# Optimization experiments

Hardware: AMD Instinct MI355X
Metric: run time of the kernel (lower is better)

The kernel has to match this reference:

```python
import jax, jax.numpy as jnp
import numpy as np

WS = 8            # window_size
SHIFT = WS // 2   # cyclic shift
NHEADS = 6
EPS = 1e-5


def _rel_pos_index(ws):
    coords = np.stack(np.meshgrid(np.arange(ws), np.arange(ws), indexing='ij'))  # [2,ws,ws]
    flat = coords.reshape(2, -1)                       # [2,N]
    rel = flat[:, :, None] - flat[:, None, :]          # [2,N,N]
    rel = rel.transpose(1, 2, 0).copy()
    rel[:, :, 0] += ws - 1
    rel[:, :, 1] += ws - 1
    rel[:, :, 0] *= 2 * ws - 1
    return rel.sum(-1)                                 # [N,N] indices into bias table


def _attn_mask(H, W, ws, shift):
    # standard Swin boundary mask for the shifted configuration
    img = np.zeros((H, W))
    cnt = 0
    for hs in (slice(0, -ws), slice(-ws, -shift), slice(-shift, None)):
        for wsl in (slice(0, -ws), slice(-ws, -shift), slice(-shift, None)):
            img[hs, wsl] = cnt
            cnt += 1
    mw = img.reshape(H // ws, ws, W // ws, ws).transpose(0, 2, 1, 3).reshape(-1, ws * ws)
    m = mw[:, None, :] - mw[:, :, None]
    return np.where(m != 0, -100.0, 0.0).astype(np.float32)  # [nW, N, N]


def instance_norm(x):
    # InstanceNorm over spatial dims, no affine (torch default)
    m = x.mean(axis=(2, 3), keepdims=True)
    v = x.var(axis=(2, 3), keepdims=True)
    return (x - m) * jax.lax.rsqrt(v + EPS)


def setup_inputs() -> dict:
    key = jax.random.key(0)
    ks = jax.random.split(key, 8)
    B, C, H, W, E = 4, 192, 256, 256, 128
    s = 0.02
    return {
        'x': jax.random.normal(ks[0], (B, C, H, W), jnp.float32),
        'cond': jax.random.normal(ks[1], (B, E), jnp.float32),
        'qkv_w': jax.random.normal(ks[2], (3 * C, C), jnp.float32) * s,
        'qkv_b': jnp.zeros((3 * C,), jnp.float32),
        'proj_w': jax.random.normal(ks[3], (C, C), jnp.float32) * s,
        'proj_b': jnp.zeros((C,), jnp.float32),
        'rel_bias': jax.random.normal(ks[4], ((2 * WS - 1) ** 2, NHEADS), jnp.float32) * s,
        'film_w': jax.random.normal(ks[5], (2 * C, E), jnp.float32) * s,
        'film_b': jnp.zeros((2 * C,), jnp.float32),
    }


def shifted_window_attention(xn, qkv_w, qkv_b, proj_w, proj_b, rel_bias):
    B, C, H, W = xn.shape
    h, ws, shift = NHEADS, WS, SHIFT
    d = C // h
    N = ws * ws
    nW = (H // ws) * (W // ws)
    scale = d ** -0.5

    xs = jnp.transpose(xn, (0, 2, 3, 1))                         # BHWC
    xs = jnp.roll(xs, (-shift, -shift), axis=(1, 2))             # cyclic shift
    win = xs.reshape(B, H // ws, ws, W // ws, ws, C)
    win = win.transpose(0, 1, 3, 2, 4, 5).reshape(B * nW, N, C)  # window partition

    qkv = win @ qkv_w.T + qkv_b                                  # [Bn, N, 3C]
    q, k, v = [t.reshape(B * nW, N, h, d).transpose(0, 2, 1, 3)
               for t in jnp.split(qkv, 3, axis=-1)]              # [Bn, h, N, d]

    attn = jnp.einsum('bhnd,bhmd->bhnm', q, k) * scale           # [Bn, h, N, N]
    bias = rel_bias[_rel_pos_index(ws)].transpose(2, 0, 1)       # [h, N, N]
    attn = attn + bias[None]
    mask = jnp.asarray(_attn_mask(H, W, ws, shift))              # [nW, N, N]
    attn = attn.reshape(B, nW, h, N, N) + mask[None, :, None]
    attn = jax.nn.softmax(attn, axis=-1).reshape(B * nW, h, N, N)

    out = jnp.einsum('bhnm,bhmd->bhnd', attn, v)                 # [Bn, h, N, d]
    out = out.transpose(0, 2, 1, 3).reshape(B * nW, N, C)
    out = out @ proj_w.T + proj_b

    out = out.reshape(B, H // ws, W // ws, ws, ws, C)
    out = out.transpose(0, 1, 3, 2, 4, 5).reshape(B, H, W, C)    # window merge
    out = jnp.roll(out, (shift, shift), axis=(1, 2))             # reverse shift
    return jnp.transpose(out, (0, 3, 1, 2))                      # BCHW


def reference(x, cond, qkv_w, qkv_b, proj_w, proj_b, rel_bias, film_w, film_b):
    # branch 1: x + attn(norm1(x))
    xn = instance_norm(x)
    x = x + shifted_window_attention(xn, qkv_w, qkv_b, proj_w, proj_b, rel_bias)
    # branch 2: x + FiLM(norm2(x), cond)
    x2 = instance_norm(x)
    gb = cond @ film_w.T + film_b                                # [B, 2C]
    gamma, beta = jnp.split(gb, 2, axis=-1)
    x2 = x2 * gamma[:, :, None, None] + beta[:, :, None, None]
    return x + x2
```

## Files before the change

kernel.cpp:

```cpp
#include <hip/hip_runtime.h>

#define BATCH 4
#define CH    192
#define PLANE 65536

typedef unsigned short u16;
typedef unsigned char  u8;
typedef __bf16 bf16x8_t __attribute__((ext_vector_type(8)));
typedef unsigned short u16x8 __attribute__((ext_vector_type(8)));
typedef unsigned short u16x4 __attribute__((ext_vector_type(4)));
typedef float f32x4 __attribute__((ext_vector_type(4)));

__device__ __forceinline__ u16 f2bf(float f) {
  __bf16 h = (__bf16)f;
  return __builtin_bit_cast(u16, h);
}
__device__ __forceinline__ float bf2f(u16 h) {
  unsigned u = ((unsigned)h) << 16;
  return __builtin_bit_cast(float, u);
}
__device__ __forceinline__ f32x4 mfma16(u16x8 a, u16x8 b, f32x4 c) {
  return __builtin_amdgcn_mfma_f32_16x16x32_bf16(
      __builtin_bit_cast(bf16x8_t, a), __builtin_bit_cast(bf16x8_t, b), c, 0, 0, 0);
}

__global__ __launch_bounds__(256) void prep_kernel(
    const float* __restrict__ x, u16* __restrict__ xraw, float2* __restrict__ part1)
{
  __shared__ u16 tile[32*264];
  const int t = threadIdx.x;
  const int bid = blockIdx.x;
  const int cc = bid % 6;
  const int wh = (bid/6) % 32;
  const int b  = bid / 192;
  const int c0 = cc*32;
  const int ww = t >> 3, ax = t & 7;
  const int gx = (ww*8 + ax + 4) & 255;
  const int gxb = gx & ~3, gxr = gx & 3;
  const long wid = b*1024 + wh*32 + ww;

  const int scl = t >> 3, sseg = t & 7;
  float myS = 0.f, myQ = 0.f;

  for (int ay = 0; ay < 8; ++ay) {
    const int gy = (wh*8 + ay + 4) & 255;
    for (int it = 0; it < 8; ++it) {
      const int id = it*256 + t;
      const int cl = id >> 6;
      const int px = (id & 63) << 2;
      float4 v = *(const float4*)(x + (((long)(b*192+c0+cl)) << 16) + gy*256 + px);
      u16x4 pk;
      pk[0] = f2bf(v.x); pk[1] = f2bf(v.y); pk[2] = f2bf(v.z); pk[3] = f2bf(v.w);
      *(u16x4*)&tile[cl*264 + (px ^ ((cl&7)<<2))] = pk;
    }
    __syncthreads();
    {
      const int sw = (scl & 7) << 2;
      #pragma unroll
      for (int k = 0; k < 32; k += 4) {
        const int px = sseg*32 + k;
        u16x4 pv = *(const u16x4*)&tile[scl*264 + (px ^ sw)];
        float a0 = bf2f(pv[0]), a1 = bf2f(pv[1]), a2 = bf2f(pv[2]), a3 = bf2f(pv[3]);
        myS += a0 + a1 + a2 + a3;
        myQ += a0*a0 + a1*a1 + a2*a2 + a3*a3;
      }
    }
    u16* dst = xraw + wid*12288 + (ay*8+ax)*192 + c0;
    #pragma unroll
    for (int k = 0; k < 4; ++k) {
      u16x8 pk;
      #pragma unroll
      for (int e = 0; e < 8; ++e) {
        const int c = k*8 + e;
        pk[e] = tile[c*264 + (gxb ^ ((c&7)<<2)) + gxr];
      }
      *(u16x8*)(dst + k*8) = pk;
    }
    __syncthreads();
  }
  for (int off = 1; off < 8; off <<= 1) {
    myS += __shfl_xor(myS, off, 64);
    myQ += __shfl_xor(myQ, off, 64);
  }
  if (sseg == 0) {
    float2 pr = {myS, myQ};
    part1[((b*32 + wh)*6 + cc)*32 + scl] = pr;
  }
}

__global__ __launch_bounds__(256) void setup_kernel(
    const float* __restrict__ a, const float* __restrict__ b2,
    const float* __restrict__ rb, const float* __restrict__ cond,
    const float* __restrict__ fw, const float* __restrict__ fb,
    const float2* __restrict__ part1,
    u16* __restrict__ wa, u16* __restrict__ wb, u16* __restrict__ bq,
    float* __restrict__ gb, float* __restrict__ st)
{
  const int blk = blockIdx.x;
  if (blk < 432) {
    const int i = blk*256 + threadIdx.x;
    if (i < 576*192) wa[i] = f2bf(a[i]);
    if (i < 192*192) wb[i] = f2bf(b2[i]);
    if (i < 1350) bq[i] = f2bf(rb[i]);
  } else if (blk < 438) {
    const int i = (blk - 432)*256 + threadIdx.x;
    if (i >= BATCH*384) return;
    const int bb = i / 384, oc = i - bb*384;
    const float* cw = fw + oc*128;
    const float* cv = cond + bb*128;
    float s = fb[oc];
    for (int k = 0; k < 128; ++k) s += cv[k]*cw[k];
    gb[i] = s;
  } else {
    const int i = (blk - 438)*256 + threadIdx.x;
    if (i >= 768) return;
    const int b = i / 192, c = i % 192;
    const int cg = c >> 5, cl = c & 31;
    float s = 0.f, q = 0.f;
    for (int wh = 0; wh < 32; ++wh) {
      float2 v = part1[((b*32 + wh)*6 + cg)*32 + cl];
      s += v.x; q += v.y;
    }
    const float mean = s * (1.f/PLANE);
    const float var  = q * (1.f/PLANE) - mean*mean;
    st[i*2]   = mean;
    st[i*2+1] = rsqrtf(var + 1e-5f);
  }
}

__global__ __launch_bounds__(512, 4) void attn_kernel(
    const u16* __restrict__ xn, const u16* __restrict__ wq, const u16* __restrict__ wp,
    const float* __restrict__ qkvb, const float* __restrict__ projb,
    const u16* __restrict__ bq, const float* __restrict__ st,
    u16* __restrict__ pw, float2* __restrict__ part)
{
  __shared__ __attribute__((aligned(16))) unsigned char smem[76624];
  u16*    Xs    = (u16*)smem;
  u16*    G     = (u16*)(smem + 25600);
  u16*    Vt    = (u16*)(smem + 43008);
  u16*    Pout  = (u16*)(smem + 25600);
  u16*    biasB = (u16*)(smem + 52224);
  float2* stpNp = (float2*)(smem + 54928);
  float2* stpR  = (float2*)(smem + 56656);
  u16*    Ps    = (u16*)(smem + 58192);

  const int t    = threadIdx.x;
  const int lane = t & 63;
  const int wave = t >> 6;
  const int arow = lane & 15;
  const int kgrp = lane >> 4;

  const int bid = blockIdx.x;
  const int wid = (bid & 7) * 512 + (bid >> 3);
  const int b   = wid >> 10;
  const int wh  = (wid >> 5) & 31;
  const int ww  = wid & 31;

  for (int i = t; i < 1350; i += 512) biasB[i] = bq[i];
  if (t < 192) {
    const float mean = st[(b*192 + t)*2];
    const float rstd = st[(b*192 + t)*2 + 1];
    float2 n = {mean, rstd};
    float2 r = {mean, 1.0f / rstd};
    stpNp[t + (t >> 3)] = n;
    stpR[t] = r;
  }
  __syncthreads();

  const u16* src = xn + (long)wid*12288;
  #pragma unroll
  for (int it = 0; it < 3; ++it) {
    const int id = it*512 + t;
    const int row = id/24, c8 = (id%24)*8;
    const int sbase = c8 + (c8 >> 3);
    u16x8 raw = *(const u16x8*)(src + id*8);
    u16x8 nrm;
    #pragma unroll
    for (int e = 0; e < 8; ++e) {
      float2 mr = stpNp[sbase + e];
      nrm[e] = f2bf((bf2f(raw[e]) - mr.x) * mr.y);
    }
    *(u16x8*)&Xs[row*200 + c8] = nrm;
  }
  __syncthreads();

  const int hh = wave >> 2;
  const int mt = wave & 3;
  const bool boundary = (wh == 31) || (ww == 31);
  u16x4 og[3][2];

  #pragma unroll
  for (int g = 0; g < 3; ++g) {
    for (int nt0 = wave; nt0 < 12; nt0 += 8) {
      f32x4 acc[4] = {{0,0,0,0},{0,0,0,0},{0,0,0,0},{0,0,0,0}};
      const int col = nt0*16 + arow;
      const int mat = col >> 6;
      const int ch  = mat*192 + g*64 + (col & 63);
      const u16* wrow = wq + ch*192 + kgrp*8;
      #pragma unroll
      for (int ks = 0; ks < 6; ++ks) {
        u16x8 bfr = *(const u16x8*)(wrow + ks*32);
        #pragma unroll
        for (int m = 0; m < 4; ++m) {
          u16x8 af = *(const u16x8*)&Xs[(m*16+arow)*200 + ks*32 + kgrp*8];
          acc[m] = mfma16(af, bfr, acc[m]);
        }
      }
      const float addb = qkvb[ch];
      if (mat == 2) {
        const int vc = col & 63;
        #pragma unroll
        for (int m = 0; m < 4; ++m) {
          u16x4 pk;
          #pragma unroll
          for (int r = 0; r < 4; ++r) pk[r] = f2bf(acc[m][r] + addb);
          *(u16x4*)&Vt[vc*72 + m*16 + kgrp*4] = pk;
        }
      } else {
        const float mult = (mat == 0) ? 0.17677669529663687f : 1.0f;
        const int gc = mat*64 + (col & 63);
        #pragma unroll
        for (int m = 0; m < 4; ++m)
          #pragma unroll
          for (int r = 0; r < 4; ++r)
            G[(m*16 + kgrp*4 + r)*136 + gc] = f2bf((acc[m][r] + addb)*mult);
      }
    }
    __syncthreads();

    const int hd = g*2 + hh;
    u16x8 qf = *(const u16x8*)&G[(mt*16+arow)*136 + hh*32 + kgrp*8];
    f32x4 sv[4];
    #pragma unroll
    for (int nt = 0; nt < 4; ++nt) {
      u16x8 kf = *(const u16x8*)&G[(nt*16+arow)*136 + 64 + hh*32 + kgrp*8];
      f32x4 z = {0,0,0,0};
      sv[nt] = mfma16(qf, kf, z);
    }

    int qj6[4];
    #pragma unroll
    for (int nt = 0; nt < 4; ++nt) {
      const int j = nt*16 + arow;
      qj6[nt] = ((j>>3)*15 + (j&7))*6;
    }
    float p[4][4];
    if (!boundary) {
      #pragma unroll
      for (int r = 0; r < 4; ++r) {
        const int i = mt*16 + kgrp*4 + r;
        const int qib = ((i>>3)*15 + (i&7) + 112)*6 + hd;
        #pragma unroll
        for (int nt = 0; nt < 4; ++nt)
          p[nt][r] = sv[nt][r] + bf2f(biasB[qib - qj6[nt]]);
      }
    } else {
      #pragma unroll
      for (int r = 0; r < 4; ++r) {
        const int i  = mt*16 + kgrp*4 + r;
        const int iy = i >> 3, ix = i & 7;
        const int qib = (iy*15 + ix + 112)*6 + hd;
        const int ri = ((wh==31) ? (iy<4?1:2) : 0)*3 + ((ww==31) ? (ix<4?1:2) : 0);
        #pragma unroll
        for (int nt = 0; nt < 4; ++nt) {
          const int j  = nt*16 + arow;
          const int jy = j >> 3, jx = j & 7;
          const int rj = ((wh==31) ? (jy<4?1:2) : 0)*3 + ((ww==31) ? (jx<4?1:2) : 0);
          float sc = sv[nt][r] + bf2f(biasB[qib - qj6[nt]]);
          if (ri != rj) sc -= 100.0f;
          p[nt][r] = sc;
        }
      }
    }
    #pragma unroll
    for (int r = 0; r < 4; ++r) {
      float sum = 0.f;
      #pragma unroll
      for (int nt = 0; nt < 4; ++nt) { p[nt][r] = __expf(p[nt][r]); sum += p[nt][r]; }
      for (int off = 1; off < 16; off <<= 1) sum += __shfl_xor(sum, off, 64);
      const float inv = 1.0f / sum;
      #pragma unroll
      for (int nt = 0; nt < 4; ++nt) p[nt][r] *= inv;
    }
    u16* myP = Ps + wave*1152;
    #pragma unroll
    for (int r = 0; r < 4; ++r) {
      const int i = kgrp*4 + r;
      #pragma unroll
      for (int nt = 0; nt < 4; ++nt) {
        const int j = nt*16 + arow;
        myP[i*72 + ((j + 8*i) & 63)] = f2bf(p[nt][r]);
      }
    }
    f32x4 oacc[2] = {{0,0,0,0},{0,0,0,0}};
    #pragma unroll
    for (int ks = 0; ks < 2; ++ks) {
      u16x8 pf = *(const u16x8*)&myP[arow*72 + ((ks*32 + kgrp*8 + 8*arow) & 63)];
      #pragma unroll
      for (int nt = 0; nt < 2; ++nt) {
        u16x8 vf = *(const u16x8*)&Vt[(hh*32 + nt*16 + arow)*72 + ks*32 + kgrp*8];
        oacc[nt] = mfma16(pf, vf, oacc[nt]);
      }
    }
    #pragma unroll
    for (int nt = 0; nt < 2; ++nt)
      #pragma unroll
      for (int r = 0; r < 4; ++r)
        og[g][nt][r] = f2bf(oacc[nt][r]);
    __syncthreads();
  }

  u16x8 rawreg[3];
  #pragma unroll
  for (int it = 0; it < 3; ++it) {
    const int id = it*512 + t;
    const int c = id >> 3, tk8 = (id & 7)*8;
    const float2 mi = stpR[c];
    u16x8 rr;
    #pragma unroll
    for (int e = 0; e < 8; ++e) {
      float nv = bf2f(Xs[(tk8 + e)*200 + c]);
      rr[e] = f2bf(nv*mi.y + mi.x);
    }
    rawreg[it] = rr;
  }
  __syncthreads();

  #pragma unroll
  for (int g = 0; g < 3; ++g)
    #pragma unroll
    for (int nt = 0; nt < 2; ++nt) {
      const int colb = g*64 + hh*32 + nt*16 + arow;
      #pragma unroll
      for (int r = 0; r < 4; ++r)
        Xs[(mt*16 + kgrp*4 + r)*200 + colb] = og[g][nt][r];
    }
  __syncthreads();

  for (int nt0 = wave; nt0 < 12; nt0 += 8) {
    const int ch = nt0*16 + arow;
    const float pb = projb[ch];
    f32x4 acc[4];
    #pragma unroll
    for (int m = 0; m < 4; ++m) { f32x4 v = {pb,pb,pb,pb}; acc[m] = v; }
    const u16* wrow = wp + ch*192 + kgrp*8;
    #pragma unroll
    for (int ks = 0; ks < 6; ++ks) {
      u16x8 bfr = *(const u16x8*)(wrow + ks*32);
      #pragma unroll
      for (int m = 0; m < 4; ++m) {
        u16x8 af = *(const u16x8*)&Xs[(m*16+arow)*200 + ks*32 + kgrp*8];
        acc[m] = mfma16(af, bfr, acc[m]);
      }
    }
    #pragma unroll
    for (int m = 0; m < 4; ++m) {
      u16x4 pk;
      #pragma unroll
      for (int r = 0; r < 4; ++r) pk[r] = f2bf(acc[m][r]);
      *(u16x4*)&Pout[ch*72 + m*16 + kgrp*4] = pk;
    }
  }
  __syncthreads();

  u16* dstw = pw + (long)wid*12288;
  #pragma unroll
  for (int it = 0; it < 3; ++it) {
    const int id = it*512 + t;
    const int c = id >> 3, tk8 = (id & 7)*8;
    u16x8 pv = *(const u16x8*)&Pout[c*72 + tk8];
    u16x8 rr = rawreg[it];
    u16x8 vb;
    float s = 0.f, q = 0.f;
    #pragma unroll
    for (int e = 0; e < 8; ++e) {
      float v = bf2f(rr[e]) + bf2f(pv[e]);
      vb[e] = f2bf(v);
      s += v; q += v*v;
    }
    *(u16x8*)(dstw + c*64 + tk8) = vb;
    s += __shfl_xor(s, 1, 64); q += __shfl_xor(q, 1, 64);
    s += __shfl_xor(s, 2, 64); q += __shfl_xor(q, 2, 64);
    s += __shfl_xor(s, 4, 64); q += __shfl_xor(q, 4, 64);
    if ((lane & 7) == 0) {
      float2 pr = {s, q};
      part[(long)wid*192 + c] = pr;
    }
  }
}

__global__ __launch_bounds__(256) void stats2_kernel(
    const float2* __restrict__ part, float2* __restrict__ st2f) {
  const int b = blockIdx.x / 12, cg = blockIdx.x % 12;
  const int cl = threadIdx.x & 15;
  const int w0 = threadIdx.x >> 4;
  const int c = cg*16 + cl;
  float s = 0.f, q = 0.f;
  for (int w = w0; w < 1024; w += 16) {
    float2 v = part[((long)(b*1024 + w))*192 + c];
    s += v.x; q += v.y;
  }
  s += __shfl_xor(s, 16, 64); q += __shfl_xor(q, 16, 64);
  s += __shfl_xor(s, 32, 64); q += __shfl_xor(q, 32, 64);
  __shared__ float2 aux[4][16];
  if ((threadIdx.x & 63) < 16) { float2 v = {s, q}; aux[threadIdx.x >> 6][cl] = v; }
  __syncthreads();
  if (threadIdx.x < 16) {
    float2 a0 = aux[0][cl], a1 = aux[1][cl], a2 = aux[2][cl], a3 = aux[3][cl];
    float S = a0.x + a1.x + a2.x + a3.x;
    float Q = a0.y + a1.y + a2.y + a3.y;
    float mean = S * (1.f/PLANE);
    float var  = Q * (1.f/PLANE) - mean*mean;
    float2 o = {mean, rsqrtf(var + 1e-5f)};
    st2f[b*192 + c] = o;
  }
}

__global__ __launch_bounds__(256) void final_kernel(
    const u16* __restrict__ pw, const float2* __restrict__ st2f,
    const float* __restrict__ gb, float* __restrict__ out)
{
  __shared__ u16 tile[32*264];
  const int t = threadIdx.x;
  const int bid = blockIdx.x;
  const int lin = (bid & 7)*96 + (bid >> 3);
  const int cc = lin % 6;
  const int band = lin / 6;
  const int wh = band & 31;
  const int b  = band >> 5;
  const int c0 = cc*32;

  const int ww = t >> 3, cq = t & 7;
  const long wid = b*1024 + wh*32 + ww;
  const u16* srcw = pw + wid*12288;
  const int g1 = ww*8 + 4, g2 = (ww*8 + 8) & 255;

  const int cl = t >> 3, seg = t & 7;
  const int c = c0 + cl;
  const float2 mr = st2f[b*192 + c];
  const float mean = mr.x, rstd = mr.y;
  const float gmm  = gb[b*384 + c];
  const float be   = gb[b*384 + 192 + c];
  const int swb = (cl & 7) << 2;

  for (int ay = 0; ay < 8; ++ay) {
    #pragma unroll
    for (int j = 0; j < 4; ++j) {
      const int ca = cq*4 + j;
      u16x8 v = *(const u16x8*)(srcw + (c0+ca)*64 + ay*8);
      const int sw = (ca & 7) << 2;
      u16x4 lo = {v[0],v[1],v[2],v[3]}, hi = {v[4],v[5],v[6],v[7]};
      *(u16x4*)&tile[ca*264 + (g1 ^ sw)] = lo;
      *(u16x4*)&tile[ca*264 + (g2 ^ sw)] = hi;
    }
    __syncthreads();

    const int gy = (wh*8 + ay + 4) & 255;
    const long base = (((long)(b*192 + c)) << 16) + gy*256 + seg*32;
    float* orow = out + base;
    #pragma unroll
    for (int q4 = 0; q4 < 32; q4 += 4) {
      const int px = seg*32 + q4;
      u16x4 pv = *(const u16x4*)&tile[cl*264 + (px ^ swb)];
      float4 o;
      float v0 = bf2f(pv[0]), v1 = bf2f(pv[1]), v2 = bf2f(pv[2]), v3 = bf2f(pv[3]);
      o.x = v0 + (v0 - mean)*rstd*gmm + be;
      o.y = v1 + (v1 - mean)*rstd*gmm + be;
      o.z = v2 + (v2 - mean)*rstd*gmm + be;
      o.w = v3 + (v3 - mean)*rstd*gmm + be;
      *(float4*)(orow + q4) = o;
    }
    __syncthreads();
  }
}

extern "C" void kernel_launch(void* const* d_in, const int* in_sizes, int n_in,
                              void* d_out, int out_size, void* d_ws, size_t ws_size,
                              hipStream_t stream) {
  const float* x      = (const float*)d_in[0];
  const float* cond   = (const float*)d_in[1];
  const float* qkv_w  = (const float*)d_in[2];
  const float* qkv_b  = (const float*)d_in[3];
  const float* proj_w = (const float*)d_in[4];
  const float* proj_b = (const float*)d_in[5];
  const float* relb   = (const float*)d_in[6];
  const float* film_w = (const float*)d_in[7];
  const float* film_b = (const float*)d_in[8];
  float* out = (float*)d_out;

  char* ws = (char*)d_ws;
  float*  stats1 = (float*)ws;
  float2* st2f   = (float2*)(ws + 6144);
  float*  gb     = (float*)(ws + 12288);
  u16*    wq     = (u16*)(ws + 18432);
  u16*    wp     = (u16*)(ws + 239616);
  u16*    bqq    = (u16*)(ws + 313344);
  u16*    xbuf   = (u16*)(ws + 362496);
  float2* part   = (float2*)(ws + 362496 + 100663296);
  float2* part1  = (float2*)(ws + 362496 + 100663296 + 6291456);

  prep_kernel<<<768, 256, 0, stream>>>(x, xbuf, part1);
  setup_kernel<<<441, 256, 0, stream>>>(qkv_w, proj_w, relb, cond, film_w, film_b,
                                        part1, wq, wp, bqq, gb, stats1);
  attn_kernel<<<4096, 512, 0, stream>>>(xbuf, wq, wp, qkv_b, proj_b, bqq, stats1, xbuf, part);
  stats2_kernel<<<48, 256, 0, stream>>>(part, st2f);
  final_kernel<<<768, 256, 0, stream>>>(xbuf, st2f, gb, out);
}
```

Baseline: 470.2 us.

## Fold instance-norm statistics into per-batch QKV weights and bias

Instead of normalizing each window's input in the attention kernel, the per-channel rstd is folded into a per-batch copy of the QKV weight, and the mean term into a per-batch bias, computed by a new small kernel. The attention kernel then loads raw bf16 input directly into shared memory, and the residual path reuses the raw values without de-normalizing. This removes per-element normalize and de-normalize arithmetic, plus the stats tables in LDS, from the hot kernel. In exchange it adds an extra launch, a four-times larger weight footprint in cache, and bf16 rounding of the scaled weights, with the mean subtraction now done in fp32 against unnormalized inputs.

```diff
diff --git a/kernel.cpp b/kernel.cpp
--- a/kernel.cpp
+++ b/kernel.cpp
@@ -5,7 +5,6 @@
 #define PLANE 65536
 
 typedef unsigned short u16;
-typedef unsigned char  u8;
 typedef __bf16 bf16x8_t __attribute__((ext_vector_type(8)));
 typedef unsigned short u16x8 __attribute__((ext_vector_type(8)));
 typedef unsigned short u16x4 __attribute__((ext_vector_type(4)));
@@ -89,21 +88,19 @@
 }
 
 __global__ __launch_bounds__(256) void setup_kernel(
-    const float* __restrict__ a, const float* __restrict__ b2,
-    const float* __restrict__ rb, const float* __restrict__ cond,
-    const float* __restrict__ fw, const float* __restrict__ fb,
-    const float2* __restrict__ part1,
-    u16* __restrict__ wa, u16* __restrict__ wb, u16* __restrict__ bq,
+    const float* __restrict__ b2, const float* __restrict__ rb,
+    const float* __restrict__ cond, const float* __restrict__ fw,
+    const float* __restrict__ fb, const float2* __restrict__ part1,
+    u16* __restrict__ wb, u16* __restrict__ bq,
     float* __restrict__ gb, float* __restrict__ st)
 {
   const int blk = blockIdx.x;
-  if (blk < 432) {
+  if (blk < 144) {
     const int i = blk*256 + threadIdx.x;
-    if (i < 576*192) wa[i] = f2bf(a[i]);
     if (i < 192*192) wb[i] = f2bf(b2[i]);
     if (i < 1350) bq[i] = f2bf(rb[i]);
-  } else if (blk < 438) {
-    const int i = (blk - 432)*256 + threadIdx.x;
+  } else if (blk < 150) {
+    const int i = (blk - 144)*256 + threadIdx.x;
     if (i >= BATCH*384) return;
     const int bb = i / 384, oc = i - bb*384;
     const float* cw = fw + oc*128;
@@ -112,7 +109,7 @@
     for (int k = 0; k < 128; ++k) s += cv[k]*cw[k];
     gb[i] = s;
   } else {
-    const int i = (blk - 438)*256 + threadIdx.x;
+    const int i = (blk - 150)*256 + threadIdx.x;
     if (i >= 768) return;
     const int b = i / 192, c = i % 192;
     const int cg = c >> 5, cl = c & 31;
@@ -128,21 +125,42 @@
   }
 }
 
+__global__ __launch_bounds__(256) void wtrans_kernel(
+    const float* __restrict__ qkv_w, const float* __restrict__ qkv_b,
+    const float* __restrict__ st, u16* __restrict__ wqb, float* __restrict__ qkvbT)
+{
+  const int blk = blockIdx.x;
+  if (blk < 1728) {
+    const int i = blk*256 + threadIdx.x;
+    const int b = i / 110592;
+    const int rem = i - b*110592;
+    const int k = rem % 192;
+    const float rstd = st[(b*192 + k)*2 + 1];
+    wqb[i] = f2bf(qkv_w[rem] * rstd);
+  } else {
+    const int j = (blk - 1728)*256 + threadIdx.x;
+    if (j >= 2304) return;
+    const int b = j / 576, ch = j - b*576;
+    const float* wr = qkv_w + ch*192;
+    const float* stb = st + b*384;
+    float s = 0.f;
+    for (int k = 0; k < 192; ++k) s += wr[k] * stb[2*k+1] * stb[2*k];
+    qkvbT[j] = qkv_b[ch] - s;
+  }
+}
+
 __global__ __launch_bounds__(512, 4) void attn_kernel(
-    const u16* __restrict__ xn, const u16* __restrict__ wq, const u16* __restrict__ wp,
-    const float* __restrict__ qkvb, const float* __restrict__ projb,
-    const u16* __restrict__ bq, const float* __restrict__ st,
-    u16* __restrict__ pw, float2* __restrict__ part)
+    const u16* __restrict__ xn, const u16* __restrict__ wqb, const u16* __restrict__ wp,
+    const float* __restrict__ qkvbT, const float* __restrict__ projb,
+    const u16* __restrict__ bq, u16* __restrict__ pw, float2* __restrict__ part)
 {
-  __shared__ __attribute__((aligned(16))) unsigned char smem[76624];
+  __shared__ __attribute__((aligned(16))) unsigned char smem[73360];
   u16*    Xs    = (u16*)smem;
   u16*    G     = (u16*)(smem + 25600);
   u16*    Vt    = (u16*)(smem + 43008);
   u16*    Pout  = (u16*)(smem + 25600);
   u16*    biasB = (u16*)(smem + 52224);
-  float2* stpNp = (float2*)(smem + 54928);
-  float2* stpR  = (float2*)(smem + 56656);
-  u16*    Ps    = (u16*)(smem + 58192);
+  u16*    Ps    = (u16*)(smem + 54928);
 
   const int t    = threadIdx.x;
   const int lane = t & 63;
@@ -156,31 +174,17 @@
   const int wh  = (wid >> 5) & 31;
   const int ww  = wid & 31;
 
+  const u16*   wqB = wqb + (long)b*110592;
+  const float* qbT = qkvbT + b*576;
+
   for (int i = t; i < 1350; i += 512) biasB[i] = bq[i];
-  if (t < 192) {
-    const float mean = st[(b*192 + t)*2];
-    const float rstd = st[(b*192 + t)*2 + 1];
-    float2 n = {mean, rstd};
-    float2 r = {mean, 1.0f / rstd};
-    stpNp[t + (t >> 3)] = n;
-    stpR[t] = r;
-  }
-  __syncthreads();
 
   const u16* src = xn + (long)wid*12288;
   #pragma unroll
   for (int it = 0; it < 3; ++it) {
     const int id = it*512 + t;
     const int row = id/24, c8 = (id%24)*8;
-    const int sbase = c8 + (c8 >> 3);
-    u16x8 raw = *(const u16x8*)(src + id*8);
-    u16x8 nrm;
-    #pragma unroll
-    for (int e = 0; e < 8; ++e) {
-      float2 mr = stpNp[sbase + e];
-      nrm[e] = f2bf((bf2f(raw[e]) - mr.x) * mr.y);
-    }
-    *(u16x8*)&Xs[row*200 + c8] = nrm;
+    *(u16x8*)&Xs[row*200 + c8] = *(const u16x8*)(src + id*8);
   }
   __syncthreads();
 
@@ -196,7 +200,7 @@
       const int col = nt0*16 + arow;
       const int mat = col >> 6;
       const int ch  = mat*192 + g*64 + (col & 63);
-      const u16* wrow = wq + ch*192 + kgrp*8;
+      const u16* wrow = wqB + ch*192 + kgrp*8;
       #pragma unroll
       for (int ks = 0; ks < 6; ++ks) {
         u16x8 bfr = *(const u16x8*)(wrow + ks*32);
@@ -206,7 +210,7 @@
           acc[m] = mfma16(af, bfr, acc[m]);
         }
       }
-      const float addb = qkvb[ch];
+      const float addb = qbT[ch];
       if (mat == 2) {
         const int vc = col & 63;
         #pragma unroll
@@ -315,13 +319,10 @@
   for (int it = 0; it < 3; ++it) {
     const int id = it*512 + t;
     const int c = id >> 3, tk8 = (id & 7)*8;
-    const float2 mi = stpR[c];
     u16x8 rr;
     #pragma unroll
-    for (int e = 0; e < 8; ++e) {
-      float nv = bf2f(Xs[(tk8 + e)*200 + c]);
-      rr[e] = f2bf(nv*mi.y + mi.x);
-    }
+    for (int e = 0; e < 8; ++e)
+      rr[e] = Xs[(tk8 + e)*200 + c];
     rawreg[it] = rr;
   }
   __syncthreads();
@@ -492,17 +493,19 @@
   float*  stats1 = (float*)ws;
   float2* st2f   = (float2*)(ws + 6144);
   float*  gb     = (float*)(ws + 12288);
-  u16*    wq     = (u16*)(ws + 18432);
-  u16*    wp     = (u16*)(ws + 239616);
-  u16*    bqq    = (u16*)(ws + 313344);
-  u16*    xbuf   = (u16*)(ws + 362496);
-  float2* part   = (float2*)(ws + 362496 + 100663296);
-  float2* part1  = (float2*)(ws + 362496 + 100663296 + 6291456);
+  u16*    wp     = (u16*)(ws + 18432);
+  u16*    bqq    = (u16*)(ws + 92160);
+  float*  qkvbT  = (float*)(ws + 94864);
+  u16*    wqb    = (u16*)(ws + 104080);
+  u16*    xbuf   = (u16*)(ws + 988816);
+  float2* part   = (float2*)(ws + 988816 + 100663296);
+  float2* part1  = (float2*)(ws + 988816 + 100663296 + 6291456);
 
   prep_kernel<<<768, 256, 0, stream>>>(x, xbuf, part1);
-  setup_kernel<<<441, 256, 0, stream>>>(qkv_w, proj_w, relb, cond, film_w, film_b,
-                                        part1, wq, wp, bqq, gb, stats1);
-  attn_kernel<<<4096, 512, 0, stream>>>(xbuf, wq, wp, qkv_b, proj_b, bqq, stats1, xbuf, part);
+  setup_kernel<<<153, 256, 0, stream>>>(proj_w, relb, cond, film_w, film_b,
+                                        part1, wp, bqq, gb, stats1);
+  wtrans_kernel<<<1737, 256, 0, stream>>>(qkv_w, qkv_b, stats1, wqb, qkvbT);
+  attn_kernel<<<4096, 512, 0, stream>>>(xbuf, wqb, wp, qkvbT, proj_b, bqq, xbuf, part);
   stats2_kernel<<<48, 256, 0, stream>>>(part, st2f);
   final_kernel<<<768, 256, 0, stream>>>(xbuf, st2f, gb, out);
 }
```

After: 491.5 us. +4.5%, slower.
